# Performance work log

Measured on AMD Instinct MI355X. Metric: run time of the kernel, lower is better.

Reference implementation:

```python
import jax, jax.numpy as jnp
import numpy as np

N = 50000
NEG_SLOPE = 0.2


def gat_conv(x, src, dst, W, al, ar, b, res=None, activation=None):
    # x: [N, F_in]; W: [F_in, H*D]; al, ar: [H, D]; b: [H*D]
    H, D = al.shape
    h = (x @ W).reshape(-1, H, D)                      # [N, H, D]
    el = jnp.sum(h * al, axis=-1)                      # [N, H]
    er = jnp.sum(h * ar, axis=-1)                      # [N, H]
    e = jax.nn.leaky_relu(el[src] + er[dst], NEG_SLOPE)  # [E, H]
    # edge softmax grouped by destination node
    m = jax.ops.segment_max(e, dst, num_segments=N)    # [N, H]
    ex = jnp.exp(e - m[dst])
    s = jax.ops.segment_sum(ex, dst, num_segments=N)   # [N, H]
    alpha = ex / s[dst]                                # [E, H]
    msg = h[src] * alpha[..., None]                    # [E, H, D]
    out = jax.ops.segment_sum(msg, dst, num_segments=N)  # [N, H, D]
    if res is not None:
        if res is True:  # identity residual (F_in == H*D)
            out = out + x.reshape(-1, H, D)
        else:            # projected residual, res: [F_in, H*D]
            out = out + (x @ res).reshape(-1, H, D)
    out = out + b.reshape(1, H, D)
    if activation is not None:
        out = activation(out)
    return out


def setup_inputs() -> dict:
    key = jax.random.key(0)
    ks = jax.random.split(key, 16)
    E = 800000
    IN, HID, CLS, H = 256, 64, 32, 2
    x = jax.random.normal(ks[0], (N, IN), dtype=jnp.float32)
    edge_src = jax.random.randint(ks[1], (E,), 0, N, dtype=jnp.int32)
    edge_dst = jax.random.randint(ks[2], (E,), 0, N, dtype=jnp.int32)

    def lin(k, fi, fo):
        return jax.random.normal(k, (fi, fo), dtype=jnp.float32) * (1.0 / np.sqrt(fi))

    W0 = lin(ks[3], IN, H * HID)
    al0 = jax.random.normal(ks[4], (H, HID), dtype=jnp.float32) * 0.1
    ar0 = jax.random.normal(ks[5], (H, HID), dtype=jnp.float32) * 0.1
    b0 = jnp.zeros((H * HID,), dtype=jnp.float32)
    W1 = lin(ks[6], H * HID, H * HID)
    al1 = jax.random.normal(ks[7], (H, HID), dtype=jnp.float32) * 0.1
    ar1 = jax.random.normal(ks[8], (H, HID), dtype=jnp.float32) * 0.1
    b1 = jnp.zeros((H * HID,), dtype=jnp.float32)
    W2 = lin(ks[9], H * HID, H * CLS)
    al2 = jax.random.normal(ks[10], (H, CLS), dtype=jnp.float32) * 0.1
    ar2 = jax.random.normal(ks[11], (H, CLS), dtype=jnp.float32) * 0.1
    b2 = jnp.zeros((H * CLS,), dtype=jnp.float32)
    Wres2 = lin(ks[12], H * HID, H * CLS)
    return {"x": x, "edge_src": edge_src, "edge_dst": edge_dst,
            "W0": W0, "al0": al0, "ar0": ar0, "b0": b0,
            "W1": W1, "al1": al1, "ar1": ar1, "b1": b1,
            "W2": W2, "al2": al2, "ar2": ar2, "b2": b2,
            "Wres2": Wres2}


def reference(x, edge_src, edge_dst, W0, al0, ar0, b0, W1, al1, ar1, b1,
              W2, al2, ar2, b2, Wres2):
    elu = jax.nn.elu
    h = gat_conv(x, edge_src, edge_dst, W0, al0, ar0, b0,
                 res=None, activation=elu)
    h = h.reshape(h.shape[0], -1)  # flatten heads: [N, H*D]
    h = gat_conv(h, edge_src, edge_dst, W1, al1, ar1, b1,
                 res=True, activation=elu)  # identity residual
    h = h.reshape(h.shape[0], -1)
    h = gat_conv(h, edge_src, edge_dst, W2, al2, ar2, b2,
                 res=Wres2, activation=None)  # [N, H, CLS]
    logits = h.mean(axis=1)  # mean over heads -> [N, CLS]
    return logits
```

## Files before the change

### kernel.cpp

```cpp
#include <hip/hip_runtime.h>
#include <math.h>


typedef unsigned int uint;
typedef unsigned short ushort;
typedef __attribute__((ext_vector_type(8))) short bf16x8;
typedef __attribute__((ext_vector_type(4))) float f32x4;

#define NBK 196
#define BCAP 4608

__device__ inline uint f2bf(float f) {
    uint u = __float_as_uint(f);
    return (u + 0x7fffu + ((u >> 16) & 1u)) >> 16;
}

__device__ inline uint4 pack8(float4 a, float4 b) {
    return make_uint4(f2bf(a.x) | (f2bf(a.y) << 16), f2bf(a.z) | (f2bf(a.w) << 16),
                      f2bf(b.x) | (f2bf(b.y) << 16), f2bf(b.z) | (f2bf(b.w) << 16));
}

__global__ __launch_bounds__(256) void buildA_k(
    const int* __restrict__ src, const int* __restrict__ dst, int E,
    int* __restrict__ bcur, uint* __restrict__ bdata, int nba,
    const float* __restrict__ W0, const float* __restrict__ W1,
    const float* __restrict__ W2, const float* __restrict__ Wr,
    ushort* __restrict__ Wt0, ushort* __restrict__ Wt1,
    ushort* __restrict__ Wt2cat) {
    __shared__ int lhist[NBK];
    __shared__ int gbase[NBK];
    const int t = threadIdx.x;
    if ((int)blockIdx.x >= nba) {
        int wb = blockIdx.x - nba;
        if (wb < 128) {
            int i = wb * 256 + t;
            int n = i >> 8, k = i & 255;
            Wt0[n * 256 + k] = (ushort)f2bf(W0[k * 128 + n]);
        } else if (wb < 192) {
            int i = (wb - 128) * 256 + t;
            int n = i >> 7, k = i & 127;
            Wt1[n * 128 + k] = (ushort)f2bf(W1[k * 128 + n]);
        } else if (wb < 224) {
            int i = (wb - 192) * 256 + t;
            int n = i >> 7, k = i & 127;
            Wt2cat[n * 128 + k] = (ushort)f2bf(W2[k * 64 + n]);
        } else {
            int i = (wb - 224) * 256 + t;
            int n = i >> 7, k = i & 127;
            Wt2cat[(64 + n) * 128 + k] = (ushort)f2bf(Wr[k * 64 + n]);
        }
        return;
    }
    for (int i = t; i < NBK; i += 256) lhist[i] = 0;
    __syncthreads();
    const int e0 = blockIdx.x * 2048 + t * 8;
    uint payload[8], meta[8];
#pragma unroll
    for (int i = 0; i < 8; ++i) {
        int e = e0 + i;
        if (e < E) {
            int s = src[e], d = dst[e];
            int b = d >> 8;
            int r = atomicAdd(&lhist[b], 1);
            payload[i] = ((uint)s << 8) | (uint)(d & 255);
            meta[i] = ((uint)b << 16) | (uint)r;
        } else {
            meta[i] = 0xffffffffu;
        }
    }
    __syncthreads();
    for (int i = t; i < NBK; i += 256) {
        int c = lhist[i];
        gbase[i] = c ? atomicAdd(&bcur[i], c) : 0;
    }
    __syncthreads();
#pragma unroll
    for (int i = 0; i < 8; ++i) {
        if (meta[i] != 0xffffffffu) {
            int b = meta[i] >> 16;
            int pos = gbase[b] + (int)(meta[i] & 0xffffu);
            if (pos < BCAP) bdata[(size_t)b * BCAP + pos] = payload[i];
        }
    }
}

__device__ void bucketB_body(
    float* smemf, int b, const uint* __restrict__ bdata,
    const int* __restrict__ bcur, int* __restrict__ deg,
    int* __restrict__ offs, int* __restrict__ ssrc, int n,
    int* __restrict__ meta, int* __restrict__ nl0, int* __restrict__ nl1,
    int* __restrict__ nl2) {
    int* lhist = (int*)smemf;
    int* lofs  = lhist + 256;
    int* lcur  = lofs + 256;
    int* stmp  = lcur + 256;
    int* lc    = stmp + 256;
    int* lb    = lc + 3;
    int* sgb   = lb + 3;
    const int t = threadIdx.x;
    const int cnt = min(bcur[b], BCAP);
    int cv = (t < NBK) ? min(bcur[t], BCAP) : 0;
    stmp[t] = cv;
    lhist[t] = 0;
    if (t < 3) lc[t] = 0;
    __syncthreads();
    for (int o = 1; o < 256; o <<= 1) {
        int add = (t >= o) ? stmp[t - o] : 0;
        __syncthreads();
        stmp[t] += add;
        __syncthreads();
    }
    if (t == 0) sgb[0] = b ? stmp[b - 1] : 0;
    __syncthreads();
    const int gb = sgb[0];
    const uint* bd = bdata + (size_t)b * BCAP;
    for (int i = t; i < cnt; i += 256)
        atomicAdd(&lhist[bd[i] & 255], 1);
    __syncthreads();
    int v = lhist[t];
    stmp[t] = v;
    __syncthreads();
    for (int o = 1; o < 256; o <<= 1) {
        int add = (t >= o) ? stmp[t - o] : 0;
        __syncthreads();
        stmp[t] += add;
        __syncthreads();
    }
    lofs[t] = stmp[t] - v;
    lcur[t] = 0;
    __syncthreads();
    int node = b * 256 + t;
    int cls = -1, r = 0;
    if (node < n) {
        deg[node] = v;
        offs[node] = gb + lofs[t];
        cls = (v <= 16) ? 0 : ((v <= 32) ? 1 : 2);
        r = atomicAdd(&lc[cls], 1);
    }
    __syncthreads();
    if (t < 3) lb[t] = lc[t] ? atomicAdd(&meta[t], lc[t]) : 0;
    __syncthreads();
    if (node < n) {
        int* nl = (cls == 0) ? nl0 : ((cls == 1) ? nl1 : nl2);
        nl[lb[cls] + r] = node;
    }
    for (int i = t; i < cnt; i += 256) {
        uint p = bd[i];
        int dl = p & 255;
        int rr = atomicAdd(&lcur[dl], 1);
        ssrc[gb + lofs[dl] + rr] = (int)(p >> 8);
    }
}

template <int K, bool L2MODE, bool AFP32>
__device__ void gemm_body(
    float* smem, const float* __restrict__ Af, const ushort* __restrict__ Ab,
    const ushort* __restrict__ Wt, ushort* __restrict__ Hb,
    float* __restrict__ hres, int nrows,
    const float* __restrict__ al, const float* __restrict__ ar,
    float* __restrict__ el, float* __restrict__ er, int bid) {
    constexpr int WS = 136;
    ushort* Ws = (ushort*)smem;
    float* Cs = smem;
    float* alr = smem + 8704;
    const int tid = threadIdx.x;
    const int w = tid >> 6;
    const int lane = tid & 63;
    const int l15 = lane & 15, quad = lane >> 4;
    const int w2 = w >> 1;
    const int wc = w & 1;
    const int row0 = bid * 64;
    constexpr int NC = L2MODE ? 64 : 128;

    if (tid < 2 * NC) alr[tid] = (tid < NC) ? al[tid] : ar[tid - NC];

    const int ar0i = row0 + w2 * 32 + l15;
    const bool av0 = ar0i < nrows;
    const bool av1 = ar0i + 16 < nrows;

    f32x4 acc[2][4];
#pragma unroll
    for (int m = 0; m < 2; ++m)
#pragma unroll
        for (int i = 0; i < 4; ++i) acc[m][i] = (f32x4){0.f, 0.f, 0.f, 0.f};

    union BC { uint4 u; bf16x8 b; };

#pragma unroll
    for (int kh = 0; kh < K / 128; ++kh) {
        if (kh) __syncthreads();
#pragma unroll
        for (int t = 0; t < 8; ++t) {
            int idx = tid + t * 256;
            int n = idx >> 4, c8 = idx & 15;
            *(uint4*)&Ws[n * WS + c8 * 8] =
                *(const uint4*)&Wt[(size_t)n * K + kh * 128 + c8 * 8];
        }
        __syncthreads();
#pragma unroll
        for (int ks = 0; ks < 4; ++ks) {
            const int kc = kh * 128 + ks * 32 + quad * 8;
            bf16x8 af0 = {0, 0, 0, 0, 0, 0, 0, 0};
            bf16x8 af1 = {0, 0, 0, 0, 0, 0, 0, 0};
            if (AFP32) {
                if (av0) {
                    float4 v0 = *(const float4*)&Af[(size_t)ar0i * K + kc];
                    float4 v1 = *(const float4*)&Af[(size_t)ar0i * K + kc + 4];
                    BC cu; cu.u = pack8(v0, v1); af0 = cu.b;
                }
                if (av1) {
                    float4 v0 = *(const float4*)&Af[(size_t)(ar0i + 16) * K + kc];
                    float4 v1 = *(const float4*)&Af[(size_t)(ar0i + 16) * K + kc + 4];
                    BC cu; cu.u = pack8(v0, v1); af1 = cu.b;
                }
            } else {
                if (av0) af0 = *(const bf16x8*)&Ab[(size_t)ar0i * K + kc];
                if (av1) af1 = *(const bf16x8*)&Ab[(size_t)(ar0i + 16) * K + kc];
            }
#pragma unroll
            for (int ct = 0; ct < 4; ++ct) {
                bf16x8 bf = *(const bf16x8*)&Ws[(wc * 64 + ct * 16 + l15) * WS +
                                                ks * 32 + quad * 8];
                acc[0][ct] = __builtin_amdgcn_mfma_f32_16x16x32_bf16(af0, bf, acc[0][ct], 0, 0, 0);
                acc[1][ct] = __builtin_amdgcn_mfma_f32_16x16x32_bf16(af1, bf, acc[1][ct], 0, 0, 0);
            }
        }
    }
    __syncthreads();

#pragma unroll
    for (int m = 0; m < 2; ++m)
#pragma unroll
        for (int ct = 0; ct < 4; ++ct)
#pragma unroll
            for (int r = 0; r < 4; ++r)
                Cs[(w2 * 32 + m * 16 + quad * 4 + r) * 132 +
                   wc * 64 + ct * 16 + l15] = acc[m][ct][r];
    __syncthreads();

    if (L2MODE) {
#pragma unroll
        for (int t = 0; t < 2; ++t) {
            int chunk = tid + t * 256;
            int r = chunk >> 3, c8 = chunk & 7;
            int grow = row0 + r;
            if (grow < nrows) {
                float4 v0 = *(float4*)&Cs[r * 132 + c8 * 8];
                float4 v1 = *(float4*)&Cs[r * 132 + c8 * 8 + 4];
                *(uint4*)&Hb[(size_t)grow * 64 + c8 * 8] = pack8(v0, v1);
            }
        }
#pragma unroll
        for (int t = 0; t < 4; ++t) {
            int chunk = tid + t * 256;
            int r = chunk >> 4, c4 = chunk & 15;
            int grow = row0 + r;
            if (grow < nrows)
                *(float4*)&hres[(size_t)grow * 64 + c4 * 4] =
                    *(float4*)&Cs[r * 132 + 64 + c4 * 4];
        }
    } else {
#pragma unroll
        for (int t = 0; t < 4; ++t) {
            int chunk = tid + t * 256;
            int r = chunk >> 4, c8 = chunk & 15;
            int grow = row0 + r;
            if (grow < nrows) {
                float4 v0 = *(float4*)&Cs[r * 132 + c8 * 8];
                float4 v1 = *(float4*)&Cs[r * 132 + c8 * 8 + 4];
                *(uint4*)&Hb[(size_t)grow * 128 + c8 * 8] = pack8(v0, v1);
            }
        }
    }
    {
        constexpr int HD = L2MODE ? 32 : 64;
        int r = tid >> 2, hh = (tid >> 1) & 1, iser = tid & 1;
        int grow = row0 + r;
        const float* coef = alr + iser * NC + hh * HD;
        const float* crow = Cs + r * 132 + hh * HD;
        float sum = 0.f;
#pragma unroll
        for (int i = 0; i < HD; ++i) sum += crow[i] * coef[i];
        if (grow < nrows) (iser ? er : el)[grow * 2 + hh] = sum;
    }
}

template <int K, bool L2MODE, bool AFP32>
__global__ __launch_bounds__(256) void gemm_m(
    const float* __restrict__ Af, const ushort* __restrict__ Ab,
    const ushort* __restrict__ Wt, ushort* __restrict__ Hb,
    float* __restrict__ hres, int nrows,
    const float* __restrict__ al, const float* __restrict__ ar,
    float* __restrict__ el, float* __restrict__ er) {
    __shared__ float smem[8960];
    gemm_body<K, L2MODE, AFP32>(smem, Af, Ab, Wt, Hb, hres, nrows, al, ar,
                                el, er, blockIdx.x);
}

__global__ __launch_bounds__(256) void gemm0_bucketB_k(
    const float* __restrict__ x, const ushort* __restrict__ Wt0,
    ushort* __restrict__ Hb, int nrows,
    const float* __restrict__ al, const float* __restrict__ ar,
    float* __restrict__ el, float* __restrict__ er, int gblk,
    const uint* __restrict__ bdata, const int* __restrict__ bcur,
    int* __restrict__ deg, int* __restrict__ offs, int* __restrict__ ssrc,
    int* __restrict__ meta, int* __restrict__ nl0, int* __restrict__ nl1,
    int* __restrict__ nl2) {
    __shared__ float smem[8960];
    if ((int)blockIdx.x < gblk) {
        gemm_body<256, false, true>(smem, x, nullptr, Wt0, Hb, nullptr, nrows,
                                    al, ar, el, er, blockIdx.x);
    } else {
        bucketB_body(smem, blockIdx.x - gblk, bdata, bcur, deg, offs, ssrc,
                     nrows, meta, nl0, nl1, nl2);
    }
}

template <int D, bool MEAN_HEADS, bool RES_BF16, int LPN>
__device__ __forceinline__ void agg_group(
    int node, int lane, float2* __restrict__ wlsw,
    const int* __restrict__ ssrc, const int* __restrict__ offs,
    const int* __restrict__ deg, const ushort* __restrict__ hb,
    const float* __restrict__ el, const float* __restrict__ er,
    const float* __restrict__ bias, const void* __restrict__ res,
    float* __restrict__ out, ushort* __restrict__ outb, int act) {
    constexpr int F = 2 * D;
    constexpr int CH = F / 8;
    constexpr int ESL = LPN / CH;
    constexpr int UB = 8;
    static_assert(ESL >= 1, "LPN must cover a full row");
    const int g = lane / LPN, sl = lane % LPN;
    const bool valid = node >= 0;
    float2* wls = wlsw + g * (LPN * 2);
    int off = 0, dg = 0;
    float2 ern = make_float2(0.f, 0.f);
    if (valid) {
        off = offs[node];
        dg = deg[node];
        ern = *(const float2*)&er[node * 2];
    }
    const uint4* __restrict__ hp = (const uint4*)hb;
    const int c = sl & (CH - 1);
    const int es = sl / CH;
    const int h1 = (c >= CH / 2) ? 1 : 0;
    const float2* wbase = wls + es * 2 + h1;
    float acc[8];
#pragma unroll
    for (int i = 0; i < 8; ++i) acc[i] = 0.f;

    auto inner = [&](int cnt) {
        for (int p = 0; p < cnt; p += UB * ESL) {
            float2 mw[UB];
#pragma unroll
            for (int u = 0; u < UB; ++u) mw[u] = wbase[(p + u * ESL) * 2];
            uint4 q[UB];
#pragma unroll
            for (int u = 0; u < UB; ++u)
                q[u] = hp[(size_t)__float_as_int(mw[u].x) * CH + c];
#pragma unroll
            for (int u = 0; u < UB; ++u) {
                float wj = mw[u].y;
                acc[0] += wj * __uint_as_float(q[u].x << 16);
                acc[1] += wj * __uint_as_float(q[u].x & 0xffff0000u);
                acc[2] += wj * __uint_as_float(q[u].y << 16);
                acc[3] += wj * __uint_as_float(q[u].y & 0xffff0000u);
                acc[4] += wj * __uint_as_float(q[u].z << 16);
                acc[5] += wj * __uint_as_float(q[u].z & 0xffff0000u);
                acc[6] += wj * __uint_as_float(q[u].w << 16);
                acc[7] += wj * __uint_as_float(q[u].w & 0xffff0000u);
            }
        }
    };

    bool big = false;
    if constexpr (LPN == 64) big = (dg > 64);

    if (!big) {
        int sidx = 0;
        float a = -INFINITY, b = -INFINITY;
        if (valid && sl < dg) {
            sidx = ssrc[off + sl];
            float2 ev = *(const float2*)&el[sidx * 2];
            a = ev.x + ern.x; a = fmaxf(a, 0.2f * a);
            b = ev.y + ern.y; b = fmaxf(b, 0.2f * b);
        }
        float m0 = a, m1 = b;
#pragma unroll
        for (int o = LPN / 2; o; o >>= 1) {
            m0 = fmaxf(m0, __shfl_xor(m0, o));
            m1 = fmaxf(m1, __shfl_xor(m1, o));
        }
        float p0 = (valid && sl < dg) ? __expf(a - m0) : 0.f;
        float p1 = (valid && sl < dg) ? __expf(b - m1) : 0.f;
        float s0 = p0, s1 = p1;
#pragma unroll
        for (int o = LPN / 2; o; o >>= 1) {
            s0 += __shfl_xor(s0, o);
            s1 += __shfl_xor(s1, o);
        }
        float is0 = s0 > 0.f ? 1.f / s0 : 0.f;
        float is1 = s1 > 0.f ? 1.f / s1 : 0.f;
        wls[sl * 2 + 0] = make_float2(__int_as_float(sidx), p0 * is0);
        wls[sl * 2 + 1] = make_float2(__int_as_float(sidx), p1 * is1);
        inner(dg);
    } else if constexpr (LPN == 64) {
        float s0 = 0.f, s1 = 0.f;
        float m0 = -INFINITY, m1 = -INFINITY;
        for (int k = sl; k < dg; k += 64) {
            int sidx = ssrc[off + k];
            float2 ev = *(const float2*)&el[sidx * 2];
            float a = ev.x + ern.x; a = fmaxf(a, 0.2f * a);
            float b = ev.y + ern.y; b = fmaxf(b, 0.2f * b);
            float nm = fmaxf(m0, a);
            s0 = s0 * __expf(m0 - nm) + __expf(a - nm); m0 = nm;
            nm = fmaxf(m1, b);
            s1 = s1 * __expf(m1 - nm) + __expf(b - nm); m1 = nm;
        }
        for (int o = 32; o; o >>= 1) {
            float om = __shfl_xor(m0, o), os = __shfl_xor(s0, o);
            float nm = fmaxf(m0, om);
            s0 = (nm == -INFINITY) ? 0.f : s0 * __expf(m0 - nm) + os * __expf(om - nm);
            m0 = nm;
            om = __shfl_xor(m1, o); os = __shfl_xor(s1, o);
            nm = fmaxf(m1, om);
            s1 = (nm == -INFINITY) ? 0.f : s1 * __expf(m1 - nm) + os * __expf(om - nm);
            m1 = nm;
        }
        float is0 = s0 > 0.f ? 1.f / s0 : 0.f;
        float is1 = s1 > 0.f ? 1.f / s1 : 0.f;
        for (int cc = 0; cc < dg; cc += 64) {
            int k = cc + sl;
            int sidx = 0;
            float w0 = 0.f, w1 = 0.f;
            if (k < dg) {
                sidx = ssrc[off + k];
                float2 ev = *(const float2*)&el[sidx * 2];
                float a = ev.x + ern.x; a = fmaxf(a, 0.2f * a);
                float b = ev.y + ern.y; b = fmaxf(b, 0.2f * b);
                w0 = __expf(a - m0) * is0;
                w1 = __expf(b - m1) * is1;
            }
            wls[sl * 2 + 0] = make_float2(__int_as_float(sidx), w0);
            wls[sl * 2 + 1] = make_float2(__int_as_float(sidx), w1);
            inner(min(64, dg - cc));
        }
    }

#pragma unroll
    for (int o = CH; o < LPN; o <<= 1) {
#pragma unroll
        for (int i = 0; i < 8; ++i) acc[i] += __shfl_xor(acc[i], o);
    }
    if (!valid) return;

    const int f0 = c * 8;
    float4 b0v = *(const float4*)&bias[f0];
    float4 b1v = *(const float4*)&bias[f0 + 4];
    float vv[8] = {acc[0] + b0v.x, acc[1] + b0v.y, acc[2] + b0v.z, acc[3] + b0v.w,
                   acc[4] + b1v.x, acc[5] + b1v.y, acc[6] + b1v.z, acc[7] + b1v.w};
    if (res) {
        if (RES_BF16) {
            uint4 r = ((const uint4*)res)[(size_t)node * CH + c];
            vv[0] += __uint_as_float(r.x << 16);
            vv[1] += __uint_as_float(r.x & 0xffff0000u);
            vv[2] += __uint_as_float(r.y << 16);
            vv[3] += __uint_as_float(r.y & 0xffff0000u);
            vv[4] += __uint_as_float(r.z << 16);
            vv[5] += __uint_as_float(r.z & 0xffff0000u);
            vv[6] += __uint_as_float(r.w << 16);
            vv[7] += __uint_as_float(r.w & 0xffff0000u);
        } else {
            const float* rf = (const float*)res;
            float4 r0v = *(const float4*)&rf[(size_t)node * F + f0];
            float4 r1v = *(const float4*)&rf[(size_t)node * F + f0 + 4];
            vv[0] += r0v.x; vv[1] += r0v.y; vv[2] += r0v.z; vv[3] += r0v.w;
            vv[4] += r1v.x; vv[5] += r1v.y; vv[6] += r1v.z; vv[7] += r1v.w;
        }
    }
    if (act) {
#pragma unroll
        for (int i = 0; i < 8; ++i)
            vv[i] = vv[i] > 0.f ? vv[i] : __expf(vv[i]) - 1.f;
    }
    if (MEAN_HEADS) {
        float ov[8];
#pragma unroll
        for (int i = 0; i < 8; ++i) ov[i] = __shfl_xor(vv[i], CH / 2);
        if (es == 0 && c < CH / 2) {
            float4 u0 = make_float4(0.5f * (vv[0] + ov[0]), 0.5f * (vv[1] + ov[1]),
                                    0.5f * (vv[2] + ov[2]), 0.5f * (vv[3] + ov[3]));
            float4 u1 = make_float4(0.5f * (vv[4] + ov[4]), 0.5f * (vv[5] + ov[5]),
                                    0.5f * (vv[6] + ov[6]), 0.5f * (vv[7] + ov[7]));
            *(float4*)&out[(size_t)node * D + f0] = u0;
            *(float4*)&out[(size_t)node * D + f0 + 4] = u1;
        }
    } else if (es == 0) {
        if (out) {
            *(float4*)&out[(size_t)node * F + f0] =
                make_float4(vv[0], vv[1], vv[2], vv[3]);
            *(float4*)&out[(size_t)node * F + f0 + 4] =
                make_float4(vv[4], vv[5], vv[6], vv[7]);
        }
        if (outb) {
            *(uint4*)&outb[(size_t)node * F + f0] =
                pack8(make_float4(vv[0], vv[1], vv[2], vv[3]),
                      make_float4(vv[4], vv[5], vv[6], vv[7]));
        }
    }
}

template <int D, bool MEAN_HEADS, bool RES_BF16>
__global__ __launch_bounds__(256) void agg_c2(
    const int* __restrict__ meta, const int* __restrict__ nl0,
    const int* __restrict__ nl1, const int* __restrict__ nl2,
    const int* __restrict__ ssrc, const int* __restrict__ offs,
    const int* __restrict__ deg, const ushort* __restrict__ hb,
    const float* __restrict__ el, const float* __restrict__ er,
    const float* __restrict__ bias, const void* __restrict__ res,
    float* __restrict__ out, ushort* __restrict__ outb, int act) {
    __shared__ float2 wls_all[4][128];
    const int wid = threadIdx.x >> 6;
    const int lane = threadIdx.x & 63;
    float2* wls = wls_all[wid];
    const int c0 = meta[0], c1 = meta[1], c2 = meta[2];
    const int I0 = (c0 + 3) >> 2;
    const int I01 = I0 + ((c1 + 1) >> 1);
    const int T = I01 + c2;
    const int nW = gridDim.x * 4;
    for (int it = blockIdx.x * 4 + wid; it < T; it += nW) {
        if (it < I0) {
            int idx = it * 4 + (lane >> 4);
            int node = (idx < c0) ? nl0[idx] : -1;
            agg_group<D, MEAN_HEADS, RES_BF16, 16>(node, lane, wls, ssrc, offs,
                                                   deg, hb, el, er, bias, res,
                                                   out, outb, act);
        } else if (it < I01) {
            int idx = (it - I0) * 2 + (lane >> 5);
            int node = (idx < c1) ? nl1[idx] : -1;
            agg_group<D, MEAN_HEADS, RES_BF16, 32>(node, lane, wls, ssrc, offs,
                                                   deg, hb, el, er, bias, res,
                                                   out, outb, act);
        } else {
            int node = nl2[it - I01];
            agg_group<D, MEAN_HEADS, RES_BF16, 64>(node, lane, wls, ssrc, offs,
                                                   deg, hb, el, er, bias, res,
                                                   out, outb, act);
        }
    }
}


extern "C" void kernel_launch(void* const* d_in, const int* in_sizes, int n_in,
                              void* d_out, int out_size, void* d_ws, size_t ws_size,
                              hipStream_t stream) {
    const float* x     = (const float*)d_in[0];
    const int*   esrc  = (const int*)d_in[1];
    const int*   edst  = (const int*)d_in[2];
    const float* W0    = (const float*)d_in[3];
    const float* al0   = (const float*)d_in[4];
    const float* ar0   = (const float*)d_in[5];
    const float* b0    = (const float*)d_in[6];
    const float* W1    = (const float*)d_in[7];
    const float* al1   = (const float*)d_in[8];
    const float* ar1   = (const float*)d_in[9];
    const float* b1    = (const float*)d_in[10];
    const float* W2    = (const float*)d_in[11];
    const float* al2   = (const float*)d_in[12];
    const float* ar2   = (const float*)d_in[13];
    const float* b2    = (const float*)d_in[14];
    const float* Wres2 = (const float*)d_in[15];

    const int N = in_sizes[0] / 256;
    const int E = in_sizes[1];

    float* ws = (float*)d_ws;
    float* hres  = ws;
    float* el    = hres + (size_t)N * 64;
    float* er    = el + (size_t)N * 2;
    int* deg     = (int*)(er + (size_t)N * 2);
    int* offs    = deg + N;
    int* bcur    = offs + N;
    int* bbase   = bcur + 256;
    int* ssrc    = bbase + 256;
    uint* bdata  = (uint*)(ssrc + E);
    ushort* Hb   = (ushort*)(bdata + (size_t)NBK * BCAP);
    ushort* Ab   = Hb + (size_t)N * 128;
    ushort* Bb   = Ab + (size_t)N * 128;
    ushort* Wt0  = Bb + (size_t)N * 128;
    ushort* Wt1  = Wt0 + 128 * 256;
    ushort* Wt2c = Wt1 + 128 * 128;
    int* nl0     = (int*)(Wt2c + 128 * 128);
    int* nl1     = nl0 + N;
    int* nl2     = nl1 + N;
    int* meta    = bcur + 208;

    hipMemsetAsync(bcur, 0, 256 * sizeof(int), stream);
    const int nba = (E + 2047) / 2048;
    buildA_k<<<nba + 256, 256, 0, stream>>>(esrc, edst, E, bcur, bdata, nba,
                                            W0, W1, W2, Wres2, Wt0, Wt1, Wt2c);

    const int gblk = (N + 63) / 64;
    const int ablk = 2048;

    gemm0_bucketB_k<<<gblk + NBK, 256, 0, stream>>>(
        x, Wt0, Hb, N, al0, ar0, el, er, gblk,
        bdata, bcur, deg, offs, ssrc, meta, nl0, nl1, nl2);
    agg_c2<64, false, false><<<ablk, 256, 0, stream>>>(
        meta, nl0, nl1, nl2, ssrc, offs, deg, Hb, el, er, b0, nullptr,
        nullptr, Ab, 1);

    gemm_m<128, false, false><<<gblk, 256, 0, stream>>>(
        nullptr, Ab, Wt1, Hb, nullptr, N, al1, ar1, el, er);
    agg_c2<64, false, true><<<ablk, 256, 0, stream>>>(
        meta, nl0, nl1, nl2, ssrc, offs, deg, Hb, el, er, b1, Ab,
        nullptr, Bb, 1);

    gemm_m<128, true, false><<<gblk, 256, 0, stream>>>(
        nullptr, Bb, Wt2c, Hb, hres, N, al2, ar2, el, er);
    agg_c2<32, true, false><<<ablk, 256, 0, stream>>>(
        meta, nl0, nl1, nl2, ssrc, offs, deg, Hb, el, er, b2, hres,
        (float*)d_out, nullptr, 0);
}
```

Measured before the change: 265.2 us.

## Fuse all GAT stages into one cooperative persistent kernel with grid syncs

Result: slower. 416.5 us (+57.1%).

```diff
diff --git a/kernel.cpp b/kernel.cpp
--- a/kernel.cpp
+++ b/kernel.cpp
@@ -1,5 +1,8 @@
 #include <hip/hip_runtime.h>
+#include <hip/hip_cooperative_groups.h>
 #include <math.h>
+
+namespace cg = cooperative_groups;
 
 
 typedef unsigned int uint;
@@ -20,18 +23,18 @@
                       f2bf(b.x) | (f2bf(b.y) << 16), f2bf(b.z) | (f2bf(b.w) << 16));
 }
 
-__global__ __launch_bounds__(256) void buildA_k(
-    const int* __restrict__ src, const int* __restrict__ dst, int E,
-    int* __restrict__ bcur, uint* __restrict__ bdata, int nba,
+__device__ void buildA_body(
+    int* lds, int u, const int* __restrict__ src, const int* __restrict__ dst,
+    int E, int* __restrict__ bcur, uint* __restrict__ bdata, int nba,
     const float* __restrict__ W0, const float* __restrict__ W1,
     const float* __restrict__ W2, const float* __restrict__ Wr,
     ushort* __restrict__ Wt0, ushort* __restrict__ Wt1,
     ushort* __restrict__ Wt2cat) {
-    __shared__ int lhist[NBK];
-    __shared__ int gbase[NBK];
+    int* lhist = lds;
+    int* gbase = lds + NBK;
     const int t = threadIdx.x;
-    if ((int)blockIdx.x >= nba) {
-        int wb = blockIdx.x - nba;
+    if (u >= nba) {
+        int wb = u - nba;
         if (wb < 128) {
             int i = wb * 256 + t;
             int n = i >> 8, k = i & 255;
@@ -53,7 +56,7 @@
     }
     for (int i = t; i < NBK; i += 256) lhist[i] = 0;
     __syncthreads();
-    const int e0 = blockIdx.x * 2048 + t * 8;
+    const int e0 = u * 2048 + t * 8;
     uint payload[8], meta[8];
 #pragma unroll
     for (int i = 0; i < 8; ++i) {
@@ -82,6 +85,18 @@
             if (pos < BCAP) bdata[(size_t)b * BCAP + pos] = payload[i];
         }
     }
+}
+
+__global__ __launch_bounds__(256) void buildA_k(
+    const int* __restrict__ src, const int* __restrict__ dst, int E,
+    int* __restrict__ bcur, uint* __restrict__ bdata, int nba,
+    const float* __restrict__ W0, const float* __restrict__ W1,
+    const float* __restrict__ W2, const float* __restrict__ Wr,
+    ushort* __restrict__ Wt0, ushort* __restrict__ Wt1,
+    ushort* __restrict__ Wt2cat) {
+    __shared__ int lds[2 * NBK];
+    buildA_body(lds, blockIdx.x, src, dst, E, bcur, bdata, nba,
+                W0, W1, W2, Wr, Wt0, Wt1, Wt2cat);
 }
 
 __device__ void bucketB_body(
@@ -283,6 +298,7 @@
         for (int i = 0; i < HD; ++i) sum += crow[i] * coef[i];
         if (grow < nrows) (iser ? er : el)[grow * 2 + hh] = sum;
     }
+    __syncthreads();
 }
 
 template <int K, bool L2MODE, bool AFP32>
@@ -510,7 +526,8 @@
 }
 
 template <int D, bool MEAN_HEADS, bool RES_BF16>
-__global__ __launch_bounds__(256) void agg_c2(
+__device__ void agg_layer_body(
+    float2* wls, int wgid, int nW, int lane,
     const int* __restrict__ meta, const int* __restrict__ nl0,
     const int* __restrict__ nl1, const int* __restrict__ nl2,
     const int* __restrict__ ssrc, const int* __restrict__ offs,
@@ -518,16 +535,11 @@
     const float* __restrict__ el, const float* __restrict__ er,
     const float* __restrict__ bias, const void* __restrict__ res,
     float* __restrict__ out, ushort* __restrict__ outb, int act) {
-    __shared__ float2 wls_all[4][128];
-    const int wid = threadIdx.x >> 6;
-    const int lane = threadIdx.x & 63;
-    float2* wls = wls_all[wid];
     const int c0 = meta[0], c1 = meta[1], c2 = meta[2];
     const int I0 = (c0 + 3) >> 2;
     const int I01 = I0 + ((c1 + 1) >> 1);
     const int T = I01 + c2;
-    const int nW = gridDim.x * 4;
-    for (int it = blockIdx.x * 4 + wid; it < T; it += nW) {
+    for (int it = wgid; it < T; it += nW) {
         if (it < I0) {
             int idx = it * 4 + (lane >> 4);
             int node = (idx < c0) ? nl0[idx] : -1;
@@ -547,6 +559,85 @@
                                                    out, outb, act);
         }
     }
+}
+
+template <int D, bool MEAN_HEADS, bool RES_BF16>
+__global__ __launch_bounds__(256) void agg_c2(
+    const int* __restrict__ meta, const int* __restrict__ nl0,
+    const int* __restrict__ nl1, const int* __restrict__ nl2,
+    const int* __restrict__ ssrc, const int* __restrict__ offs,
+    const int* __restrict__ deg, const ushort* __restrict__ hb,
+    const float* __restrict__ el, const float* __restrict__ er,
+    const float* __restrict__ bias, const void* __restrict__ res,
+    float* __restrict__ out, ushort* __restrict__ outb, int act) {
+    __shared__ float2 wls_all[4][128];
+    const int wid = threadIdx.x >> 6;
+    const int lane = threadIdx.x & 63;
+    agg_layer_body<D, MEAN_HEADS, RES_BF16>(
+        wls_all[wid], blockIdx.x * 4 + wid, gridDim.x * 4, lane,
+        meta, nl0, nl1, nl2, ssrc, offs, deg, hb, el, er, bias, res,
+        out, outb, act);
+}
+
+struct MegaArgs {
+    const float* x; const int* esrc; const int* edst;
+    const float *W0, *al0, *ar0, *b0;
+    const float *W1, *al1, *ar1, *b1;
+    const float *W2, *al2, *ar2, *b2, *Wres2;
+    int N, E, nba, gblk;
+    float *hres, *el, *er;
+    int *deg, *offs, *bcur, *ssrc;
+    uint* bdata;
+    ushort *Hb, *Ab, *Bb, *Wt0, *Wt1, *Wt2c;
+    int *nl0, *nl1, *nl2, *meta;
+    float* out;
+};
+
+__global__ __launch_bounds__(256, 4) void mega_k(MegaArgs a) {
+    __shared__ float smem[8960];
+    cg::grid_group g = cg::this_grid();
+    const int nblk = gridDim.x;
+    const int wid = threadIdx.x >> 6;
+    const int lane = threadIdx.x & 63;
+    float2* wls = (float2*)smem + wid * 128;
+
+    for (int u = blockIdx.x; u < a.nba + 256; u += nblk)
+        buildA_body((int*)smem, u, a.esrc, a.edst, a.E, a.bcur, a.bdata,
+                    a.nba, a.W0, a.W1, a.W2, a.Wres2, a.Wt0, a.Wt1, a.Wt2c);
+    g.sync();
+    for (int u = blockIdx.x; u < a.gblk + NBK; u += nblk) {
+        if (u < a.gblk)
+            gemm_body<256, false, true>(smem, a.x, nullptr, a.Wt0, a.Hb,
+                                        nullptr, a.N, a.al0, a.ar0, a.el,
+                                        a.er, u);
+        else
+            bucketB_body(smem, u - a.gblk, a.bdata, a.bcur, a.deg, a.offs,
+                         a.ssrc, a.N, a.meta, a.nl0, a.nl1, a.nl2);
+    }
+    g.sync();
+    agg_layer_body<64, false, false>(wls, blockIdx.x * 4 + wid, nblk * 4,
+                                     lane, a.meta, a.nl0, a.nl1, a.nl2,
+                                     a.ssrc, a.offs, a.deg, a.Hb, a.el, a.er,
+                                     a.b0, nullptr, nullptr, a.Ab, 1);
+    g.sync();
+    for (int u = blockIdx.x; u < a.gblk; u += nblk)
+        gemm_body<128, false, false>(smem, nullptr, a.Ab, a.Wt1, a.Hb,
+                                     nullptr, a.N, a.al1, a.ar1, a.el, a.er,
+                                     u);
+    g.sync();
+    agg_layer_body<64, false, true>(wls, blockIdx.x * 4 + wid, nblk * 4,
+                                    lane, a.meta, a.nl0, a.nl1, a.nl2,
+                                    a.ssrc, a.offs, a.deg, a.Hb, a.el, a.er,
+                                    a.b1, a.Ab, nullptr, a.Bb, 1);
+    g.sync();
+    for (int u = blockIdx.x; u < a.gblk; u += nblk)
+        gemm_body<128, true, false>(smem, nullptr, a.Bb, a.Wt2c, a.Hb,
+                                    a.hres, a.N, a.al2, a.ar2, a.el, a.er, u);
+    g.sync();
+    agg_layer_body<32, true, false>(wls, blockIdx.x * 4 + wid, nblk * 4,
+                                    lane, a.meta, a.nl0, a.nl1, a.nl2,
+                                    a.ssrc, a.offs, a.deg, a.Hb, a.el, a.er,
+                                    a.b2, a.hres, a.out, nullptr, 0);
 }
 
 
@@ -594,27 +685,52 @@
     int* nl2     = nl1 + N;
     int* meta    = bcur + 208;
 
+    const int nba = (E + 2047) / 2048;
+    const int gblk = (N + 63) / 64;
+
     hipMemsetAsync(bcur, 0, 256 * sizeof(int), stream);
-    const int nba = (E + 2047) / 2048;
+
+    MegaArgs a;
+    a.x = x; a.esrc = esrc; a.edst = edst;
+    a.W0 = W0; a.al0 = al0; a.ar0 = ar0; a.b0 = b0;
+    a.W1 = W1; a.al1 = al1; a.ar1 = ar1; a.b1 = b1;
+    a.W2 = W2; a.al2 = al2; a.ar2 = ar2; a.b2 = b2; a.Wres2 = Wres2;
+    a.N = N; a.E = E; a.nba = nba; a.gblk = gblk;
+    a.hres = hres; a.el = el; a.er = er;
+    a.deg = deg; a.offs = offs; a.bcur = bcur; a.ssrc = ssrc;
+    a.bdata = bdata;
+    a.Hb = Hb; a.Ab = Ab; a.Bb = Bb; a.Wt0 = Wt0; a.Wt1 = Wt1; a.Wt2c = Wt2c;
+    a.nl0 = nl0; a.nl1 = nl1; a.nl2 = nl2; a.meta = meta;
+    a.out = (float*)d_out;
+
+    bool coop = false;
+    int nbpc = 0;
+    if (hipOccupancyMaxActiveBlocksPerMultiprocessor(
+            &nbpc, (const void*)mega_k, 256, 0) == hipSuccess && nbpc >= 1) {
+        int grid = nbpc * 256;
+        if (grid > 1024) grid = 1024;
+        void* kargs[] = {&a};
+        if (hipLaunchCooperativeKernel((const void*)mega_k, dim3(grid),
+                                       dim3(256), kargs, 0, stream) ==
+            hipSuccess)
+            coop = true;
+    }
+    if (coop) return;
+
+    const int ablk = 2048;
     buildA_k<<<nba + 256, 256, 0, stream>>>(esrc, edst, E, bcur, bdata, nba,
                                             W0, W1, W2, Wres2, Wt0, Wt1, Wt2c);
-
-    const int gblk = (N + 63) / 64;
-    const int ablk = 2048;
-
     gemm0_bucketB_k<<<gblk + NBK, 256, 0, stream>>>(
         x, Wt0, Hb, N, al0, ar0, el, er, gblk,
         bdata, bcur, deg, offs, ssrc, meta, nl0, nl1, nl2);
     agg_c2<64, false, false><<<ablk, 256, 0, stream>>>(
         meta, nl0, nl1, nl2, ssrc, offs, deg, Hb, el, er, b0, nullptr,
         nullptr, Ab, 1);
-
     gemm_m<128, false, false><<<gblk, 256, 0, stream>>>(
         nullptr, Ab, Wt1, Hb, nullptr, N, al1, ar1, el, er);
     agg_c2<64, false, true><<<ablk, 256, 0, stream>>>(
         meta, nl0, nl1, nl2, ssrc, offs, deg, Hb, el, er, b1, Ab,
         nullptr, Bb, 1);
-
     gemm_m<128, true, false><<<gblk, 256, 0, stream>>>(
         nullptr, Bb, Wt2c, Hb, hres, N, al2, ar2, el, er);
     agg_c2<32, true, false><<<ablk, 256, 0, stream>>>(
```
